# Optimization experiments

Hardware: AMD Instinct MI355X
Metric: run time of the kernel (lower is better)

The kernel has to match this reference:

```python
import jax, jax.numpy as jnp
import numpy as np

NEG = -1.0e8  # matches torch code's -100000000.0 boundary value
# state ordering: m (match)=0, x (insertion)=1, y (deletion)=2, s (slip)=3


def _viterbi_forward(theta, A):
    """Softmax-smoothed Viterbi (Forward algorithm) via anti-diagonal wavefront scan.

    theta: [N, M, S] emission potentials; A: [N, M, S, S] transition potentials (log units).
    Recurrence (original torch code):
      V[i,j,m] = lse(V[i-1,j-1] + A[i-1,j-1,m])
      V[i,j,s] = lse(V[i-1,j-1] + A[i-1,j-1,s])
      V[i,j,x] = lse(V[i-1,j  ] + A[i-1,j-1,x])
      V[i,j,y] = lse(V[i  ,j-1] + A[i-1,j-1,y])
      V[i,j] += theta[i-1,j-1];  Vt = lse(V[N,M])
    All deps of diagonal d=i+j live on diagonals d-1, d-2 -> wavefront parallel.
    """
    N, Mm, S = theta.shape
    D = N + Mm - 1  # diagonals d = 2 .. N+M hold all interior cells
    ii = jnp.arange(N + 1)                  # position along a diagonal == row index i
    dvals = jnp.arange(D)[:, None] + 2      # actual diagonal value d, shape [D,1]
    r = ii[None, :] - 1                     # theta/A row index (i-1)
    c = dvals - ii[None, :] - 1             # theta/A col index (j-1 = d-i-1)
    valid = (ii[None, :] >= 1) & (ii[None, :] <= N) & (c >= 0) & (c <= Mm - 1)
    rc = jnp.clip(r, 0, N - 1)
    cc = jnp.clip(c, 0, Mm - 1)
    theta_sk = theta[rc, cc]                # [D, N+1, S] skewed emissions
    A_sk = A[rc, cc]                        # [D, N+1, S, S] skewed transitions

    neg_row = jnp.full((1, S), NEG, theta.dtype)

    def shift(v):  # v[i] -> v[i-1], boundary row = NEG (== V[0, j] boundary)
        return jnp.concatenate([neg_row, v[:-1]], axis=0)

    V_d0 = jnp.full((N + 1, S), NEG, theta.dtype).at[0].set(0.0)  # diag d=0: V[0,0]=0
    V_d1 = jnp.full((N + 1, S), NEG, theta.dtype)                 # diag d=1: all boundary

    def step(carry, inp):
        Vd1, Vd2 = carry                    # diagonals d-1, d-2
        th_d, A_d, v_d = inp
        vdiag = shift(Vd2)                  # V[i-1, j-1]
        vup = shift(Vd1)                    # V[i-1, j]
        vleft = Vd1                         # V[i, j-1]
        # source state-vector per target state (m, x, y, s) -> [N+1, S, S]
        src = jnp.stack([vdiag, vup, vleft, vdiag], axis=1)
        new = jax.nn.logsumexp(src + A_d, axis=-1) + th_d
        new = jnp.where(v_d[:, None], new, NEG)
        return (new, Vd1), None

    (Vlast, _), _ = jax.lax.scan(step, (V_d1, V_d0), (theta_sk, A_sk, valid))
    # final diagonal d = N+M; cell (N, M) sits at index i = N
    return jax.nn.logsumexp(Vlast[N])


def setup_inputs() -> dict:
    key = jax.random.key(0)
    k1, k2 = jax.random.split(key)
    N, M, S = 1024, 1024, 4
    theta = jax.random.normal(k1, (N, M, S), dtype=jnp.float32)
    A = jax.random.normal(k2, (N, M, S, S), dtype=jnp.float32)
    return {"theta": theta, "A": A}


def reference(theta, A):
    return _viterbi_forward(theta, A)
```

## Files before the change

kernel.cpp:

```cpp
#include <hip/hip_runtime.h>
#include <stdint.h>


typedef float f32x4 __attribute__((ext_vector_type(4)));
typedef int   i32x4 __attribute__((ext_vector_type(4)));

#define MM    1024
#define LOG2E 1.4426950408889634f
#define LN2f  0.6931471805599453f
#define NEGI  (-1073741824)
#define NCH   136
#define HCT   (NCH*2)
#define DEPTH 32
#define PPS   15

#define F_RIN   0
#define F_CDONE 1
#define F_OPUB  2

__device__ __forceinline__ float ld_cohf(const float* p) {
    return __hip_atomic_load(p, __ATOMIC_RELAXED, __HIP_MEMORY_SCOPE_AGENT);
}
__device__ __forceinline__ int ld_cohi(const int* p) {
    return __hip_atomic_load(p, __ATOMIC_RELAXED, __HIP_MEMORY_SCOPE_AGENT);
}
__device__ __forceinline__ void st_cohf(float* p, float v) {
    __hip_atomic_store(p, v, __ATOMIC_RELAXED, __HIP_MEMORY_SCOPE_AGENT);
}
__device__ __forceinline__ void st_cohi(int* p, int v) {
    __hip_atomic_store(p, v, __ATOMIC_RELAXED, __HIP_MEMORY_SCOPE_AGENT);
}
__device__ __forceinline__ int lds_acq(const int* p) {
    return __hip_atomic_load(p, __ATOMIC_ACQUIRE, __HIP_MEMORY_SCOPE_WORKGROUP);
}
__device__ __forceinline__ void lds_rel(int* p, int v) {
    __hip_atomic_store(p, v, __ATOMIC_RELEASE, __HIP_MEMORY_SCOPE_WORKGROUP);
}

__device__ __forceinline__ int dpp_shr1_i(int oldv, int src) {
    return __builtin_amdgcn_update_dpp(oldv, src, 0x138, 0xF, 0xF, false);
}
__device__ __forceinline__ float dpp_shr1_f(float oldv, float src) {
    return __int_as_float(__builtin_amdgcn_update_dpp(
        __float_as_int(oldv), __float_as_int(src), 0x138, 0xF, 0xF, false));
}

#define WAITV(N) do {                                                         \
    asm volatile("s_waitcnt vmcnt(" #N ")" ::: "memory");                     \
    __builtin_amdgcn_sched_barrier(0);                                        \
} while (0)

#define ISSUE_FLAG(FX, H) do {                                                \
    const int hf_ = ((H) < HCT ? (H) : (HCT-1));                              \
    const int* rp_ = rfS + (size_t)(hf_ & (DEPTH-1)) * 16;                    \
    asm volatile("global_load_dwordx4 %0, %1, off sc0 sc1"                    \
                 : "=v"(FX) : "v"(rp_) : "memory");                           \
} while (0)

#define CHECK_FLAG(FX, H) do {                                                \
    const int hv_ = ((H) < HCT ? (H) : (HCT-1));                              \
    if (!(FX.x >= hv_ && FX.y >= hv_ && FX.z >= hv_ && FX.w >= hv_)) {        \
        const int* rp_ = rfS + (size_t)(hv_ & (DEPTH-1)) * 16;                \
        for (;;) {                                                            \
            asm volatile("global_load_dwordx4 %0, %1, off sc0 sc1\n\t"        \
                         "s_waitcnt vmcnt(0)"                                 \
                         : "=v"(FX) : "v"(rp_) : "memory");                   \
            if (FX.x >= hv_ && FX.y >= hv_ && FX.z >= hv_ && FX.w >= hv_)     \
                break;                                                        \
            __builtin_amdgcn_s_sleep(2);                                      \
        }                                                                     \
    }                                                                         \
    asm volatile("" ::: "memory");                                            \
} while (0)

#define ISSUE_DATA(PX, H) do {                                                \
    const int hcl_ = ((H) < HCT ? (H) : (HCT-1));                             \
    const char* b0_ = ringS + ((size_t)(hcl_ & (DEPTH-1)) << 14)              \
                            + (size_t)lane * 16;                              \
    const char* b1_ = b0_ + 4096;                                             \
    const char* b2_ = b0_ + 8192;                                             \
    const char* b3_ = b0_ + 12288;                                            \
    asm volatile("global_load_dwordx4 %0, %1, off sc0 sc1"              : "=v"(PX[0])  : "v"(b0_) : "memory"); \
    asm volatile("global_load_dwordx4 %0, %1, off offset:1024 sc0 sc1"  : "=v"(PX[1])  : "v"(b0_) : "memory"); \
    asm volatile("global_load_dwordx4 %0, %1, off offset:2048 sc0 sc1"  : "=v"(PX[2])  : "v"(b0_) : "memory"); \
    asm volatile("global_load_dwordx4 %0, %1, off offset:3072 sc0 sc1"  : "=v"(PX[3])  : "v"(b0_) : "memory"); \
    asm volatile("global_load_dwordx4 %0, %1, off sc0 sc1"              : "=v"(PX[4])  : "v"(b1_) : "memory"); \
    asm volatile("global_load_dwordx4 %0, %1, off offset:1024 sc0 sc1"  : "=v"(PX[5])  : "v"(b1_) : "memory"); \
    asm volatile("global_load_dwordx4 %0, %1, off offset:2048 sc0 sc1"  : "=v"(PX[6])  : "v"(b1_) : "memory"); \
    asm volatile("global_load_dwordx4 %0, %1, off offset:3072 sc0 sc1"  : "=v"(PX[7])  : "v"(b1_) : "memory"); \
    asm volatile("global_load_dwordx4 %0, %1, off sc0 sc1"              : "=v"(PX[8])  : "v"(b2_) : "memory"); \
    asm volatile("global_load_dwordx4 %0, %1, off offset:1024 sc0 sc1"  : "=v"(PX[9])  : "v"(b2_) : "memory"); \
    asm volatile("global_load_dwordx4 %0, %1, off offset:2048 sc0 sc1"  : "=v"(PX[10]) : "v"(b2_) : "memory"); \
    asm volatile("global_load_dwordx4 %0, %1, off offset:3072 sc0 sc1"  : "=v"(PX[11]) : "v"(b2_) : "memory"); \
    asm volatile("global_load_dwordx4 %0, %1, off sc0 sc1"              : "=v"(PX[12]) : "v"(b3_) : "memory"); \
    asm volatile("global_load_dwordx4 %0, %1, off offset:1024 sc0 sc1"  : "=v"(PX[13]) : "v"(b3_) : "memory"); \
    asm volatile("global_load_dwordx4 %0, %1, off offset:2048 sc0 sc1"  : "=v"(PX[14]) : "v"(b3_) : "memory"); \
    asm volatile("global_load_dwordx4 %0, %1, off offset:3072 sc0 sc1"  : "=v"(PX[15]) : "v"(b3_) : "memory"); \
} while (0)

#define CHUNKSPIN(H) do {                                                     \
    if (((H) & 1) == 0) {                                                     \
        const int cc_ = (H) >> 1;                                             \
        if (isCons) while (lds_acq(&flags[F_RIN]) < cc_) {}                   \
        if (isProd) while (lds_acq(&flags[F_OPUB]) < cc_ - 3) {}              \
    }                                                                         \
} while (0)

#define VSTEP(H, U, PX, DO_CLAMP, DO_NORM) do {                               \
    const int sb_ = (((H) >> 1) & 3) * 8 + ((H) & 1) * 4 + (U);               \
    f32x4 P0 = PX[(U)*4+0], P1 = PX[(U)*4+1];                                 \
    f32x4 P2 = PX[(U)*4+2], P3 = PX[(U)*4+3];                                 \
    int off = max(max(mD, mU), mL);                                           \
    float sd = ldexpf(1.0f, mD - off);                                        \
    float su = ldexpf(1.0f, mU - off);                                        \
    float sl = ldexpf(1.0f, mL - off);                                        \
    float dm  = fmaf(qd3,P0.w, fmaf(qd2,P0.z, fmaf(qd1,P0.y, qd0*P0.x)));     \
    float dx  = fmaf(qu3,P1.w, fmaf(qu2,P1.z, fmaf(qu1,P1.y, qu0*P1.x)));     \
    float dy  = fmaf(ql3,P2.w, fmaf(ql2,P2.z, fmaf(ql1,P2.y, ql0*P2.x)));     \
    float ds2 = fmaf(qd3,P3.w, fmaf(qd2,P3.z, fmaf(qd1,P3.y, qd0*P3.x)));     \
    float qn0 = dm*sd, qn1 = dx*su, qn2 = dy*sl, qn3 = ds2*sd;                \
    int mn = off;                                                             \
    if (DO_NORM) {                                                            \
        float gmax = fmaxf(fmaxf(qn0,qn1), fmaxf(qn2,qn3));                   \
        int e = (int)(__float_as_uint(gmax) >> 23) - 126;                     \
        qn0 = ldexpf(qn0, 1-e); qn1 = ldexpf(qn1, 1-e);                       \
        qn2 = ldexpf(qn2, 1-e); qn3 = ldexpf(qn3, 1-e);                       \
        mn = off + e - 1;                                                     \
    }                                                                         \
    if (DO_CLAMP) {                                                           \
        const int jq_ = (H)*4 + (U) - r + 1;                                  \
        const bool valid_ = (jq_ >= 1) && (jq_ <= MM);                        \
        if (!valid_) { qn0=qn1=qn2=qn3=0.f; mn=NEGI; }                        \
        if (!isProd && lane == 63 && jq_ == MM)                               \
            out[0] = LN2f * ((float)mn + log2f((qn0+qn1)+(qn2+qn3)));         \
    }                                                                         \
    if (isProd && lane == 63) {                                               \
        *(float4*)&recOut[sb_][0] = make_float4(qn0,qn1,qn2,qn3);             \
        recOut[sb_][4] = __int_as_float(mn);                                  \
    }                                                                         \
    int bmv = NEGI; float b0=0.f,b1=0.f,b2=0.f,b3=0.f;                        \
    if (isCons) {                                                             \
        float4 bb = *(const float4*)&recIn[sb_][0];                           \
        bmv = __float_as_int(recIn[sb_][4]);                                  \
        b0=bb.x; b1=bb.y; b2=bb.z; b3=bb.w;                                   \
    }                                                                         \
    mD = mU; qd0=qu0; qd1=qu1; qd2=qu2; qd3=qu3;                              \
    mU  = dpp_shr1_i(bmv, mn);                                                \
    qu0 = dpp_shr1_f(b0, qn0);                                                \
    qu1 = dpp_shr1_f(b1, qn1);                                                \
    qu2 = dpp_shr1_f(b2, qn2);                                                \
    qu3 = dpp_shr1_f(b3, qn3);                                                \
    mL = mn; ql0=qn0; ql1=qn1; ql2=qn2; ql3=qn3;                              \
} while (0)

#define CHCTAIL(H) do {                                                       \
    asm volatile("" ::: "memory");                                            \
    if (lane == 0) {                                                          \
        *(volatile int*)&flags[F_CDONE] = (H);     \
        st_cohi(cp, (H));                                 \
    }                                                                         \
} while (0)

#define COMPUTEHC_C(H, PX) do {                                               \
    VSTEP(H, 0, PX, 1, 1); VSTEP(H, 1, PX, 1, 1);                             \
    VSTEP(H, 2, PX, 1, 1); VSTEP(H, 3, PX, 1, 1);                             \
    CHCTAIL(H);                                                               \
} while (0)

#define COMPUTEHC_F(H, PX) do {                                               \
    VSTEP(H, 0, PX, 0, 0); VSTEP(H, 1, PX, 0, 1);                             \
    VSTEP(H, 2, PX, 0, 0); VSTEP(H, 3, PX, 0, 1);                             \
    CHCTAIL(H);                                                               \
} while (0)

#define CHAINBODY(H, CHC) do {                                                \
    CHUNKSPIN(H);                                                             \
    WAITV(35); CHECK_FLAG(fA, (H)+2); ISSUE_FLAG(fA, (H)+4);                  \
    WAITV(19); CHC((H), pA); ISSUE_DATA(pA, (H)+2);                           \
    WAITV(35); CHECK_FLAG(fB, (H)+3); ISSUE_FLAG(fB, (H)+5);                  \
    WAITV(19); CHC((H)+1, pB); ISSUE_DATA(pB, (H)+3);                         \
} while (0)

__global__ __launch_bounds__(256, 1) void viterbi_r14(
    const float* __restrict__ theta, const float* __restrict__ A,
    float* __restrict__ out, float* __restrict__ bnd, int* __restrict__ prog,
    int* __restrict__ cpG, int* __restrict__ rfG, float* __restrict__ ringG)
{
    __shared__ float  recIn[32][8];
    __shared__ float  recOut[32][8];
    __shared__ int    flags[16];
    extern __shared__ char dynpad[];
    (void)dynpad;

    const int tid  = threadIdx.x;
    const int wv   = tid >> 6;
    const int lane = tid & 63;
    const int bid  = blockIdx.x;

    if (tid < 16) flags[tid] = -1;
    __syncthreads();

    if (bid >= 16) {
        const int k     = bid & 7;
        const int idx   = (bid - 16) >> 3;
        const int s     = 2*k + (idx >= PPS);
        const int pslot = idx % PPS;
        const int u2    = wv;
        const int row   = s*64 + lane;
        const float4* A4 = (const float4*)A;
        const float4* T4 = (const float4*)theta;
        const int* cp = cpG + s*16;
        for (int h = pslot; h < HCT; h += PPS) {
            while (ld_cohi(cp) < h - DEPTH) __builtin_amdgcn_s_sleep(1);
            const int tau = 4*h + u2;
            int c = tau - lane; c = c < 0 ? 0 : (c > MM-1 ? MM-1 : c);
            const float4* Ar = A4 + ((size_t)row*MM + (size_t)c)*4;
            float4 a0 = Ar[0], a1 = Ar[1], a2 = Ar[2], a3 = Ar[3];
            float4 th = T4[(size_t)row*MM + (size_t)c];
            float4 p0, p1, p2, p3;
            p0.x=exp2f((a0.x+th.x)*LOG2E); p0.y=exp2f((a0.y+th.x)*LOG2E);
            p0.z=exp2f((a0.z+th.x)*LOG2E); p0.w=exp2f((a0.w+th.x)*LOG2E);
            p1.x=exp2f((a1.x+th.y)*LOG2E); p1.y=exp2f((a1.y+th.y)*LOG2E);
            p1.z=exp2f((a1.z+th.y)*LOG2E); p1.w=exp2f((a1.w+th.y)*LOG2E);
            p2.x=exp2f((a2.x+th.z)*LOG2E); p2.y=exp2f((a2.y+th.z)*LOG2E);
            p2.z=exp2f((a2.z+th.z)*LOG2E); p2.w=exp2f((a2.w+th.z)*LOG2E);
            p3.x=exp2f((a3.x+th.w)*LOG2E); p3.y=exp2f((a3.y+th.w)*LOG2E);
            p3.z=exp2f((a3.z+th.w)*LOG2E); p3.w=exp2f((a3.w+th.w)*LOG2E);
            float* dst = ringG + ((size_t)(s*DEPTH + (h & (DEPTH-1))) << 12)
                               + (size_t)((u2*4)*64 + lane)*4;
            st_cohf(dst+0,   p0.x); st_cohf(dst+1,   p0.y);
            st_cohf(dst+2,   p0.z); st_cohf(dst+3,   p0.w);
            st_cohf(dst+256, p1.x); st_cohf(dst+257, p1.y);
            st_cohf(dst+258, p1.z); st_cohf(dst+259, p1.w);
            st_cohf(dst+512, p2.x); st_cohf(dst+513, p2.y);
            st_cohf(dst+514, p2.z); st_cohf(dst+515, p2.w);
            st_cohf(dst+768, p3.x); st_cohf(dst+769, p3.y);
            st_cohf(dst+770, p3.z); st_cohf(dst+771, p3.w);
            asm volatile("s_waitcnt vmcnt(0)" ::: "memory");
            if (lane == 0)
                st_cohi(rfG + (size_t)(s*DEPTH + (h & (DEPTH-1)))*16 + u2, h);
        }
        return;
    }

    const int strip = ((bid & 7) << 1) | (bid >> 3);
    const bool isCons = (strip > 0);
    const bool isProd = (strip < 15);

    float* Prec = bnd + (size_t)strip * MM * 8;
    const float* Crec = bnd + (size_t)(strip - 1) * MM * 8;
    int* myflag = prog + strip * 32;
    const int* upflag = prog + (strip - 1) * 32;

    if (wv == 0) {
        __builtin_amdgcn_s_setprio(1);
        const int r = lane;
        int   mL = NEGI, mU = NEGI, mD = NEGI;
        float ql0=0,ql1=0,ql2=0,ql3=0;
        float qu0=0,qu1=0,qu2=0,qu3=0;
        float qd0=0,qd1=0,qd2=0,qd3=0;
        if (strip == 0 && lane == 0) { mD = 0; qd0=qd1=qd2=qd3=1.f; }
        if (isCons) {
            while (ld_cohi(upflag) < 1) __builtin_amdgcn_s_sleep(1);
            asm volatile("" ::: "memory");
            qu0 = ld_cohf(Crec+0); qu1 = ld_cohf(Crec+1);
            qu2 = ld_cohf(Crec+2); qu3 = ld_cohf(Crec+3);
            mU  = ld_cohi((const int*)Crec + 4);
        }
        int* cp = cpG + strip*16;
        const int* rfS = rfG + (size_t)strip * DEPTH * 16;
        const char* ringS = (const char*)ringG + ((size_t)strip * DEPTH << 14);
        if (lane == 0) st_cohi(cp, -1);

        f32x4 pA[16], pB[16];
        i32x4 fA = {-2,-2,-2,-2}, fB = {-2,-2,-2,-2};
        CHECK_FLAG(fA, 0); ISSUE_DATA(pA, 0);
        CHECK_FLAG(fB, 1); ISSUE_DATA(pB, 1);
        ISSUE_FLAG(fA, 2); ISSUE_FLAG(fB, 3);
        CHUNKSPIN(0);
        WAITV(1);  CHECK_FLAG(fA, 2); ISSUE_FLAG(fA, 4);
        COMPUTEHC_C(0, pA); ISSUE_DATA(pA, 2);
        WAITV(18); CHECK_FLAG(fB, 3); ISSUE_FLAG(fB, 5);
        COMPUTEHC_C(1, pB); ISSUE_DATA(pB, 3);
        for (int h = 2; h < 16; h += 2)  CHAINBODY(h, COMPUTEHC_C);
        for (int h = 16; h < 256; h += 2) CHAINBODY(h, COMPUTEHC_F);
        for (int h = 256; h < HCT; h += 2) CHAINBODY(h, COMPUTEHC_C);
    } else if (wv == 1) {
        if (!isProd) return;
        const int rec0 = lane / 5, wd0 = lane % 5;
        const int rec1 = (lane+64) / 5, wd1 = (lane+64) % 5;
        const bool on1 = (lane + 64) < 80;
        for (int cc = 0; cc < NCH; cc += 2) {
            while (lds_acq(&flags[F_CDONE]) < 2*cc + 3) __builtin_amdgcn_s_sleep(1);
            {
                int col = 8*(cc + (rec0 >> 3)) + (rec0 & 7) - 62;
                float v = recOut[(cc & 3)*8 + rec0][wd0];
                if (col >= 1 && col <= MM) st_cohf(Prec + (size_t)(col-1)*8 + wd0, v);
            }
            if (on1) {
                int col = 8*(cc + (rec1 >> 3)) + (rec1 & 7) - 62;
                float v = recOut[(cc & 3)*8 + rec1][wd1];
                if (col >= 1 && col <= MM) st_cohf(Prec + (size_t)(col-1)*8 + wd1, v);
            }
            asm volatile("s_waitcnt vmcnt(0)" ::: "memory");
            int done = 8*(cc + 1) - 55; if (done > MM) done = MM;
            if (done >= 1 && lane == 0) st_cohi(myflag, done);
            if (lane == 0) lds_rel(&flags[F_OPUB], cc + 1);
        }
    } else if (wv == 2) {
        if (!isCons) return;
        const int rec0 = lane / 5, wd0 = lane % 5;
        const int rec1 = (lane+64) / 5, wd1 = (lane+64) % 5;
        const bool on1 = (lane + 64) < 80;
        for (int cc = 0; cc < NCH; cc += 2) {
            while (lds_acq(&flags[F_CDONE]) < 2*cc - 3) __builtin_amdgcn_s_sleep(1);
            int need = 8*cc + 17; if (need > MM) need = MM;
            while (ld_cohi(upflag) < need) __builtin_amdgcn_s_sleep(1);
            asm volatile("" ::: "memory");
            {
                int col = 8*cc + 2 + rec0; if (col > MM) col = MM;
                float v = ld_cohf(Crec + (size_t)(col-1)*8 + wd0);
                recIn[(cc & 3)*8 + rec0][wd0] = v;
            }
            if (on1) {
                int col = 8*cc + 2 + rec1; if (col > MM) col = MM;
                float v = ld_cohf(Crec + (size_t)(col-1)*8 + wd1);
                recIn[(cc & 3)*8 + rec1][wd1] = v;
            }
            if (lane == 0) lds_rel(&flags[F_RIN], cc + 1);
        }
    }
}

extern "C" void kernel_launch(void* const* d_in, const int* in_sizes, int n_in,
                              void* d_out, int out_size, void* d_ws, size_t ws_size,
                              hipStream_t stream) {
    const float* theta = (const float*)d_in[0];
    const float* A     = (const float*)d_in[1];
    float* out = (float*)d_out;
    char* base = (char*)d_ws;
    float* bnd  = (float*)base;
    int*   prog = (int*)(base + (size_t)512*1024);
    int*   cpG  = (int*)(base + (size_t)512*1024 + 4*1024);
    int*   rfG  = (int*)(base + (size_t)512*1024 + 8*1024);
    float* ring = (float*)(base + (size_t)512*1024 + 64*1024);
    viterbi_r14<<<256, 256, 96*1024, stream>>>(theta, A, out, bnd, prog,
                                               cpG, rfG, ring);
}
```

Measured before the change: 608.2 us.

## Triple-buffer ring prefetch in chain wave and offload progress publishing to spare wave

The chain wavefront now keeps three in-flight prefetch buffers (pA/pB/pC) instead of two, issuing flag and data loads three half-chunks ahead to hide more global-memory latency on the serial critical path. The global progress counter store that producers poll is removed from the compute loop and handed to an otherwise idle wave, which mirrors the LDS completion flag to global memory. Producers skip the progress check for the first DEPTH slots. This raises register pressure in the chain wave and adds a small delay before producers see progress updates.

After: 642.1 us. 5.6% more time.

```diff
diff --git a/kernel.cpp b/kernel.cpp
--- a/kernel.cpp
+++ b/kernel.cpp
@@ -155,10 +155,7 @@
 
 #define CHCTAIL(H) do {                                                       \
     asm volatile("" ::: "memory");                                            \
-    if (lane == 0) {                                                          \
-        *(volatile int*)&flags[F_CDONE] = (H);     \
-        st_cohi(cp, (H));                                 \
-    }                                                                         \
+    if (lane == 0) *(volatile int*)&flags[F_CDONE] = (H);                     \
 } while (0)
 
 #define COMPUTEHC_C(H, PX) do {                                               \
@@ -173,15 +170,16 @@
     CHCTAIL(H);                                                               \
 } while (0)
 
-#define CHAINBODY(H, CHC) do {                                                \
+#define BODY3(H, PX, FX) do {                                                 \
     CHUNKSPIN(H);                                                             \
-    WAITV(35); CHECK_FLAG(fA, (H)+2); ISSUE_FLAG(fA, (H)+4);                  \
-    WAITV(19); CHC((H), pA); ISSUE_DATA(pA, (H)+2);                           \
-    WAITV(35); CHECK_FLAG(fB, (H)+3); ISSUE_FLAG(fB, (H)+5);                  \
-    WAITV(19); CHC((H)+1, pB); ISSUE_DATA(pB, (H)+3);                         \
-} while (0)
-
-__global__ __launch_bounds__(256, 1) void viterbi_r14(
+    WAITV(50); CHECK_FLAG(FX, (H)+3); ISSUE_FLAG(FX, (H)+6);                  \
+    WAITV(35);                                                                \
+    if ((H) < 16 || (H) >= 256) { COMPUTEHC_C((H), PX); }                     \
+    else                        { COMPUTEHC_F((H), PX); }                     \
+    ISSUE_DATA(PX, (H)+3);                                                    \
+} while (0)
+
+__global__ __launch_bounds__(256, 1) void viterbi_r15(
     const float* __restrict__ theta, const float* __restrict__ A,
     float* __restrict__ out, float* __restrict__ bnd, int* __restrict__ prog,
     int* __restrict__ cpG, int* __restrict__ rfG, float* __restrict__ ringG)
@@ -211,7 +209,8 @@
         const float4* T4 = (const float4*)theta;
         const int* cp = cpG + s*16;
         for (int h = pslot; h < HCT; h += PPS) {
-            while (ld_cohi(cp) < h - DEPTH) __builtin_amdgcn_s_sleep(1);
+            while (h >= DEPTH && ld_cohi(cp) < h - DEPTH)
+                __builtin_amdgcn_s_sleep(1);
             const int tau = 4*h + u2;
             int c = tau - lane; c = c < 0 ? 0 : (c > MM-1 ? MM-1 : c);
             const float4* Ar = A4 + ((size_t)row*MM + (size_t)c)*4;
@@ -267,24 +266,30 @@
             qu2 = ld_cohf(Crec+2); qu3 = ld_cohf(Crec+3);
             mU  = ld_cohi((const int*)Crec + 4);
         }
-        int* cp = cpG + strip*16;
         const int* rfS = rfG + (size_t)strip * DEPTH * 16;
         const char* ringS = (const char*)ringG + ((size_t)strip * DEPTH << 14);
-        if (lane == 0) st_cohi(cp, -1);
-
-        f32x4 pA[16], pB[16];
-        i32x4 fA = {-2,-2,-2,-2}, fB = {-2,-2,-2,-2};
+
+        f32x4 pA[16], pB[16], pC[16];
+        i32x4 fA = {-2,-2,-2,-2}, fB = {-2,-2,-2,-2}, fC = {-2,-2,-2,-2};
         CHECK_FLAG(fA, 0); ISSUE_DATA(pA, 0);
         CHECK_FLAG(fB, 1); ISSUE_DATA(pB, 1);
-        ISSUE_FLAG(fA, 2); ISSUE_FLAG(fB, 3);
+        CHECK_FLAG(fC, 2); ISSUE_DATA(pC, 2);
+        ISSUE_FLAG(fA, 3); ISSUE_FLAG(fB, 4); ISSUE_FLAG(fC, 5);
         CHUNKSPIN(0);
-        WAITV(1);  CHECK_FLAG(fA, 2); ISSUE_FLAG(fA, 4);
-        COMPUTEHC_C(0, pA); ISSUE_DATA(pA, 2);
-        WAITV(18); CHECK_FLAG(fB, 3); ISSUE_FLAG(fB, 5);
-        COMPUTEHC_C(1, pB); ISSUE_DATA(pB, 3);
-        for (int h = 2; h < 16; h += 2)  CHAINBODY(h, COMPUTEHC_C);
-        for (int h = 16; h < 256; h += 2) CHAINBODY(h, COMPUTEHC_F);
-        for (int h = 256; h < HCT; h += 2) CHAINBODY(h, COMPUTEHC_C);
+        WAITV(2);  CHECK_FLAG(fA, 3); ISSUE_FLAG(fA, 6);
+        COMPUTEHC_C(0, pA); ISSUE_DATA(pA, 3);
+        WAITV(18); CHECK_FLAG(fB, 4); ISSUE_FLAG(fB, 7);
+        COMPUTEHC_C(1, pB); ISSUE_DATA(pB, 4);
+        CHUNKSPIN(2);
+        WAITV(34); CHECK_FLAG(fC, 5); ISSUE_FLAG(fC, 8);
+        COMPUTEHC_C(2, pC); ISSUE_DATA(pC, 5);
+        for (int h = 3; h + 2 <= HCT - 3; h += 3) {
+            BODY3(h,   pA, fA);
+            BODY3(h+1, pB, fB);
+            BODY3(h+2, pC, fC);
+        }
+        BODY3(HCT-2, pA, fA);
+        BODY3(HCT-1, pB, fB);
     } else if (wv == 1) {
         if (!isProd) return;
         const int rec0 = lane / 5, wd0 = lane % 5;
@@ -329,6 +334,17 @@
             }
             if (lane == 0) lds_rel(&flags[F_RIN], cc + 1);
         }
+    } else {
+        int* cp = cpG + strip*16;
+        if (lane == 0) {
+            int last = -2;
+            for (;;) {
+                int v = lds_acq(&flags[F_CDONE]);
+                if (v != last) { st_cohi(cp, v); last = v; }
+                if (v >= HCT - 1) break;
+                __builtin_amdgcn_s_sleep(1);
+            }
+        }
     }
 }
 
@@ -344,6 +360,6 @@
     int*   cpG  = (int*)(base + (size_t)512*1024 + 4*1024);
     int*   rfG  = (int*)(base + (size_t)512*1024 + 8*1024);
     float* ring = (float*)(base + (size_t)512*1024 + 64*1024);
-    viterbi_r14<<<256, 256, 96*1024, stream>>>(theta, A, out, bnd, prog,
+    viterbi_r15<<<256, 256, 96*1024, stream>>>(theta, A, out, bnd, prog,
                                                cpG, rfG, ring);
 }
```
